# Kernel tuning notes

Hardware: AMD Instinct MI355X
Metric: run time of the kernel (lower is better)

Reference implementation:

```python
import jax, jax.numpy as jnp
import numpy as np
from jax import lax

B, N, D = 16, 4096, 64
NPOINT, RADIUS, NSAMPLE = 1024, 0.2, 32
MLP = [64, 128, 256]
IN_CH = 3 + D
EPS = 1e-5


def farthest_point_sample(xyz, npoint):
    # Deterministic FPS (start at index 0) matching the python fallback loop.
    b, n, _ = xyz.shape

    def step(carry, _):
        dist, farthest = carry
        centroid = jnp.take_along_axis(xyz, farthest[:, None, None], axis=1)  # [B,1,3]
        d = jnp.sum((xyz - centroid) ** 2, axis=-1)  # [B,N]
        dist = jnp.minimum(dist, d)
        nxt = jnp.argmax(dist, axis=-1)
        return (dist, nxt), farthest

    init = (jnp.full((b, n), 1e10, dtype=xyz.dtype), jnp.zeros((b,), jnp.int32))
    _, idx = lax.scan(step, init, None, length=npoint)
    return idx.T  # [B, npoint]


def index_points(points, idx):
    # points: [B,N,C], idx: [B,S] or [B,S,K]
    return jax.vmap(lambda p, i: p[i])(points, idx)


def square_distance(src, dst):
    # src:[B,S,C], dst:[B,N,C] -> [B,S,N]
    d = -2.0 * jnp.einsum('bsc,bnc->bsn', src, dst)
    d += jnp.sum(src ** 2, -1)[:, :, None]
    d += jnp.sum(dst ** 2, -1)[:, None, :]
    return d


def query_ball_point(radius, nsample, xyz, new_xyz):
    b, n, _ = xyz.shape
    sqrdists = square_distance(new_xyz, xyz)  # [B,S,N]
    group_idx = jnp.where(sqrdists > radius ** 2, n, jnp.arange(n, dtype=jnp.int32))
    group_idx = jnp.sort(group_idx, axis=-1)[:, :, :nsample]  # [B,S,K]
    first = group_idx[:, :, :1]
    return jnp.where(group_idx == n, first, group_idx)


def sample_and_group(npoint, radius, nsample, xyz, points):
    fps_idx = farthest_point_sample(xyz, npoint)
    new_xyz = index_points(xyz, fps_idx)  # [B,S,3]
    idx = query_ball_point(radius, nsample, xyz, new_xyz)  # [B,S,K]
    grouped_xyz = index_points(xyz, idx)  # [B,S,K,3]
    grouped_xyz_norm = grouped_xyz - new_xyz[:, :, None, :]
    grouped_points = index_points(points, idx)  # [B,S,K,D]
    new_points = jnp.concatenate([grouped_xyz_norm, grouped_points], axis=-1)
    return new_xyz, new_points


def setup_inputs() -> dict:
    key = jax.random.key(0)
    ks = jax.random.split(key, 2 + 4 * len(MLP))
    inp = {
        'xyz': jax.random.uniform(ks[0], (B, N, 3), jnp.float32),
        'points': jax.random.normal(ks[1], (B, N, D), jnp.float32),
    }
    last = IN_CH
    for i, out in enumerate(MLP):
        kw, kb = ks[2 + 4 * i], ks[3 + 4 * i]
        scale = 1.0 / np.sqrt(last)
        inp[f'w{i}'] = jax.random.normal(kw, (last, out), jnp.float32) * scale
        inp[f'b{i}'] = jax.random.normal(kb, (out,), jnp.float32) * 0.01
        inp[f'g{i}'] = jnp.ones((out,), jnp.float32)
        inp[f'bt{i}'] = jnp.zeros((out,), jnp.float32)
        last = out
    return inp


def _forward(xyz, points, params):
    new_xyz, x = sample_and_group(NPOINT, RADIUS, NSAMPLE, xyz, points)  # x:[B,S,K,C]
    for w, b, g, bt in params:
        x = jnp.einsum('bskc,cd->bskd', x, w) + b  # 1x1 Conv2d
        mean = jnp.mean(x, axis=(0, 1, 2))
        var = jnp.var(x, axis=(0, 1, 2))  # biased, as torch BN training forward
        x = jax.nn.relu((x - mean) * lax.rsqrt(var + EPS) * g + bt)
    new_points = jnp.max(x, axis=2)  # max over nsample -> [B,S,Cout]
    return new_xyz, new_points


def reference(xyz, points, w0, b0, g0, bt0, w1, b1, g1, bt1, w2, b2, g2, bt2):
    params = [(w0, b0, g0, bt0), (w1, b1, g1, bt1), (w2, b2, g2, bt2)]
    return _forward(xyz, points, params)
```

## Files before the change

kernel.cpp:

```cpp
#include <hip/hip_runtime.h>

namespace {
constexpr int kNB = 16;
constexpr int kN  = 4096;
constexpr int kD  = 64;
constexpr int kS  = 1024;
constexpr int kK  = 32;
constexpr int kG  = kNB * kS;
constexpr int C0 = 67, C1 = 64, C2 = 128, C3 = 256;
constexpr float kEps = 1e-5f;
constexpr double kR2d = 0.04000000000000001;
constexpr float kRowCount = (float)(kG * kK);
constexpr int kFT = 256;
constexpr int kFW = kFT / 64;
constexpr int kFP = kN / kFT;
constexpr int kLS = 33;
constexpr int kNF = 88;
}

typedef __attribute__((ext_vector_type(8))) short short8;
typedef __attribute__((ext_vector_type(4))) float f32x4;

__device__ __forceinline__ void split_bf16(float x, unsigned& hi, unsigned& lo) {
  const unsigned u = __float_as_uint(x);
  hi = (u + 0x7fffu + ((u >> 16) & 1u)) >> 16;
  const float rem = x - __uint_as_float(hi << 16);
  const unsigned u2 = __float_as_uint(rem);
  lo = ((u2 + 0x7fffu + ((u2 >> 16) & 1u)) >> 16) & 0xffffu;
}
__device__ __forceinline__ unsigned pack_sb(float x) {
  unsigned hi, lo;
  split_bf16(x, hi, lo);
  return (hi << 16) | lo;
}
__device__ __forceinline__ float unpack_sb(unsigned pk) {
  return __uint_as_float(pk & 0xffff0000u) + __uint_as_float(pk << 16);
}

__device__ __forceinline__ f32x4 mfma3(const short8& ah, const short8& al,
                                       const unsigned short* __restrict__ whiF,
                                       const unsigned short* __restrict__ wloF,
                                       size_t fb, f32x4 acc) {
  const short8 bh = *(const short8*)(whiF + fb);
  const short8 bl = *(const short8*)(wloF + fb);
  acc = __builtin_amdgcn_mfma_f32_16x16x32_bf16(ah, bh, acc, 0, 0, 0);
  acc = __builtin_amdgcn_mfma_f32_16x16x32_bf16(ah, bl, acc, 0, 0, 0);
  acc = __builtin_amdgcn_mfma_f32_16x16x32_bf16(al, bh, acc, 0, 0, 0);
  return acc;
}

__device__ __forceinline__ void load_afrag(const unsigned* p, int k0, int mbase,
                                           int quad, int l15, short8& hi, short8& lo) {
#pragma unroll
  for (int j = 0; j < 8; ++j) {
    const unsigned pk = p[(k0 + quad * 8 + j) * kLS + mbase + l15];
    hi[j] = (short)(pk >> 16);
    lo[j] = (short)(pk & 0xffffu);
  }
}

template <int CTRL, int RM>
__device__ __forceinline__ float dpp_max_step(float v) {
  const int vi = __float_as_int(v);
  const int sh = __builtin_amdgcn_update_dpp(vi, vi, CTRL, RM, 0xf, false);
  return fmaxf(v, __int_as_float(sh));
}
__device__ __forceinline__ float wave_max_dpp(float v) {
  v = dpp_max_step<0x111, 0xf>(v);
  v = dpp_max_step<0x112, 0xf>(v);
  v = dpp_max_step<0x114, 0xf>(v);
  v = dpp_max_step<0x118, 0xf>(v);
  v = dpp_max_step<0x142, 0xa>(v);
  v = dpp_max_step<0x143, 0xc>(v);
  return v;
}

__global__ __launch_bounds__(kFT) void fps_kernel(const float* __restrict__ xyz,
                                                  float* __restrict__ new_xyz) {
#pragma clang fp contract(off)
  const int b = blockIdx.x;
  const int tid = threadIdx.x;
  const int w = tid >> 6;
  const int lane = tid & 63;
  const float* xb = xyz + (size_t)b * kN * 3;

  __shared__ float sx[kN], sy[kN], sz[kN];
  __shared__ float sout[kS * 3];
  __shared__ float4 pV[2];
  __shared__ int4   pI[2];

  float px[kFP], py[kFP], pz[kFP], dist[kFP];
#pragma unroll
  for (int j = 0; j < kFP; ++j) {
    const int p = tid * kFP + j;
    const float x = xb[p * 3 + 0];
    const float y = xb[p * 3 + 1];
    const float z = xb[p * 3 + 2];
    px[j] = x; py[j] = y; pz[j] = z;
    sx[p] = x; sy[p] = y; sz[p] = z;
    dist[j] = 1e10f;
  }
  float cx = xb[0], cy = xb[1], cz = xb[2];
  __syncthreads();

  for (int t = 0; t < kS; ++t) {
    if (tid == 0) {
      sout[t * 3 + 0] = cx; sout[t * 3 + 1] = cy; sout[t * 3 + 2] = cz;
    }
    float lv = -1.0f;
    int bi = 0;
#pragma unroll
    for (int j = 0; j < kFP; ++j) {
      const float dx = px[j] - cx, dy = py[j] - cy, dz = pz[j] - cz;
      float d = dx * dx + dy * dy;
      d = d + dz * dz;
      const float dd = fminf(dist[j], d);
      dist[j] = dd;
      if (dd > lv) { lv = dd; bi = tid * kFP + j; }
    }
    const float wm = wave_max_dpp(lv);
    const float sM = __int_as_float(__builtin_amdgcn_readlane(__float_as_int(wm), 63));
    const unsigned long long mk = __ballot(lv == sM);
    const int fl = __builtin_ctzll(mk);
    const int cand = __builtin_amdgcn_readlane(bi, fl);
    const int par = t & 1;
    if (lane == 0) {
      ((float*)&pV[par])[w] = sM;
      ((int*)&pI[par])[w] = cand;
    }
    __syncthreads();
    const float4 vv = pV[par];
    const int4 ii = pI[par];
    float bv = vv.x; int bci = ii.x;
    if (vv.y > bv) { bv = vv.y; bci = ii.y; }
    if (vv.z > bv) { bv = vv.z; bci = ii.z; }
    if (vv.w > bv) { bv = vv.w; bci = ii.w; }
    cx = sx[bci]; cy = sy[bci]; cz = sz[bci];
  }
  __syncthreads();
  float* ob = new_xyz + (size_t)b * kS * 3;
  for (int e = tid; e < kS * 3; e += kFT) ob[e] = sout[e];
}

__global__ __launch_bounds__(256) void ball_kernel(const float* __restrict__ xyz,
                                                   const float* __restrict__ new_xyz,
                                                   int* __restrict__ idx) {
  const int g = blockIdx.x * 4 + (threadIdx.x >> 6);
  const int lane = threadIdx.x & 63;
  const int b = g >> 10;
  const float* xb = xyz + (size_t)b * kN * 3;
  const double sx = (double)new_xyz[(size_t)g * 3 + 0];
  const double sy = (double)new_xyz[(size_t)g * 3 + 1];
  const double sz = (double)new_xyz[(size_t)g * 3 + 2];
  const double s2 = sx * sx + sy * sy + sz * sz;
  int have = 0, first = -1;
  int* out = idx + (size_t)g * kK;
  for (int c = 0; c < kN; c += 64) {
    const int p = c + lane;
    const double px = (double)xb[p * 3 + 0];
    const double py = (double)xb[p * 3 + 1];
    const double pz = (double)xb[p * 3 + 2];
    const double p2 = px * px + py * py + pz * pz;
    const double dot = sx * px + sy * py + sz * pz;
    const double d = -2.0 * dot + s2 + p2;
    const bool elig = !(d > kR2d);
    const unsigned long long mask = __ballot(elig);
    if (first < 0 && mask) first = c + __builtin_ctzll(mask);
    const int pos = have + __popcll(mask & ((1ull << lane) - 1ull));
    if (elig && pos < kK) out[pos] = p;
    have += __popcll(mask);
    if (have >= kK) break;
  }
  if (have < kK) {
    if (lane >= have && lane < kK) out[lane] = first;
  }
}

__global__ __launch_bounds__(256) void wsplit_kernel(const float* __restrict__ w0,
                                                     const float* __restrict__ w1,
                                                     const float* __restrict__ w2,
                                                     unsigned short* __restrict__ whiF,
                                                     unsigned short* __restrict__ wloF) {
  const int gid = blockIdx.x * 256 + threadIdx.x;
  const int lane = gid & 63;
  const int f = gid >> 6;
  const int quad = lane >> 4, l15 = lane & 15;
  const float* src;
  int kt, nt, nstride;
  if (f < 8) { src = w0; kt = f >> 2; nt = f & 3; nstride = C1; }
  else if (f < 24) { const int fl = f - 8; src = w1; kt = fl >> 3; nt = fl & 7; nstride = C2; }
  else { const int fl = f - 24; src = w2; kt = fl >> 4; nt = fl & 15; nstride = C3; }
  const int k0 = kt * 32 + quad * 8;
  const int n = nt * 16 + l15;
#pragma unroll
  for (int j = 0; j < 8; ++j) {
    const float x = src[(size_t)(k0 + j) * nstride + n];
    unsigned hi, lo;
    split_bf16(x, hi, lo);
    whiF[(size_t)gid * 8 + j] = (unsigned short)hi;
    wloF[(size_t)gid * 8 + j] = (unsigned short)lo;
  }
}

__device__ __forceinline__ void gather_packed(int g, const float* __restrict__ xyz,
                                              const float* __restrict__ points,
                                              const float* __restrict__ new_xyz,
                                              const int* __restrict__ idx,
                                              unsigned* fsp) {
  const int b = g >> 10;
  const float* xb = xyz + (size_t)b * kN * 3;
  const float* pb = points + (size_t)b * kN * kD;
  const float nx = new_xyz[(size_t)g * 3 + 0];
  const float ny = new_xyz[(size_t)g * 3 + 1];
  const float nz = new_xyz[(size_t)g * 3 + 2];
  const int* ig = idx + (size_t)g * kK;
  for (int e = threadIdx.x; e < C0 * kK; e += 256) {
    const int c = e >> 5, r = e & 31;
    const int i = ig[r];
    float v;
    if (c == 0) v = xb[i * 3 + 0] - nx;
    else if (c == 1) v = xb[i * 3 + 1] - ny;
    else if (c == 2) v = xb[i * 3 + 2] - nz;
    else v = pb[(size_t)i * kD + (c - 3)];
    fsp[c * kLS + r] = pack_sb(v);
  }
}

__device__ __forceinline__ void l1_mfma(const unsigned* fsp,
                                        const unsigned short* __restrict__ whiF,
                                        const unsigned short* __restrict__ wloF,
                                        const float* __restrict__ w0,
                                        const float* __restrict__ b0,
                                        int mt, int nh, int quad, int l15, int lane,
                                        f32x4 out[2]) {
  short8 ah[2], al[2];
#pragma unroll
  for (int ks = 0; ks < 2; ++ks)
    load_afrag(fsp, ks * 32, mt * 16, quad, l15, ah[ks], al[ks]);
#pragma unroll
  for (int nt2 = 0; nt2 < 2; ++nt2) {
    const int nt = nh * 2 + nt2;
    const int n = nt * 16 + l15;
    f32x4 acc = {0.f, 0.f, 0.f, 0.f};
#pragma unroll
    for (int ks = 0; ks < 2; ++ks)
      acc = mfma3(ah[ks], al[ks], whiF, wloF, ((size_t)(ks * 4 + nt) * 64 + lane) * 8, acc);
#pragma unroll
    for (int c = 64; c < 67; ++c) {
      const float wv0 = w0[(size_t)c * C1 + n];
#pragma unroll
      for (int r = 0; r < 4; ++r) {
        const float x = unpack_sb(fsp[c * kLS + mt * 16 + quad * 4 + r]);
        acc[r] += x * wv0;
      }
    }
    const float bb = b0[n];
#pragma unroll
    for (int r = 0; r < 4; ++r) acc[r] += bb;
    out[nt2] = acc;
  }
}

__global__ __launch_bounds__(256) void stats1_kernel(
    const float* __restrict__ xyz, const float* __restrict__ points,
    const float* __restrict__ new_xyz, const int* __restrict__ idx,
    const float* __restrict__ w0, const float* __restrict__ b0,
    const unsigned short* __restrict__ whiF, const unsigned short* __restrict__ wloF,
    float* __restrict__ P) {
  __shared__ unsigned fsp[C0 * kLS];
  __shared__ float redS[C1 * 2], redQ[C1 * 2];
  const int g = blockIdx.x;
  const int tid = threadIdx.x;
  gather_packed(g, xyz, points, new_xyz, idx, fsp);
  __syncthreads();
  const int wv = tid >> 6, lane = tid & 63;
  const int mt = wv & 1, nh = wv >> 1;
  const int quad = lane >> 4, l15 = lane & 15;
  f32x4 acc1[2];
  l1_mfma(fsp, whiF, wloF, w0, b0, mt, nh, quad, l15, lane, acc1);
#pragma unroll
  for (int nt2 = 0; nt2 < 2; ++nt2) {
    const int n = (nh * 2 + nt2) * 16 + l15;
    const f32x4 a = acc1[nt2];
    float s = a[0] + a[1] + a[2] + a[3];
    float q = a[0] * a[0] + a[1] * a[1] + a[2] * a[2] + a[3] * a[3];
    s += __shfl_xor(s, 16); s += __shfl_xor(s, 32);
    q += __shfl_xor(q, 16); q += __shfl_xor(q, 32);
    if (quad == 0) { redS[n * 2 + mt] = s; redQ[n * 2 + mt] = q; }
  }
  __syncthreads();
  if (tid < C1) {
    P[(size_t)g * 2 * C1 + tid] = redS[tid * 2] + redS[tid * 2 + 1];
    P[(size_t)g * 2 * C1 + C1 + tid] = redQ[tid * 2] + redQ[tid * 2 + 1];
  }
}

__global__ __launch_bounds__(256) void stats2_kernel(
    const float* __restrict__ xyz, const float* __restrict__ points,
    const float* __restrict__ new_xyz, const int* __restrict__ idx,
    const float* __restrict__ w0, const float* __restrict__ b0, const float* __restrict__ ab0,
    const float* __restrict__ b1,
    const unsigned short* __restrict__ whiF, const unsigned short* __restrict__ wloF,
    float* __restrict__ P) {
  __shared__ unsigned fsp[C0 * kLS];
  __shared__ unsigned y1p[C1 * kLS];
  __shared__ float redS[C2 * 2], redQ[C2 * 2];
  const int g = blockIdx.x;
  const int tid = threadIdx.x;
  gather_packed(g, xyz, points, new_xyz, idx, fsp);
  __syncthreads();
  const int wv = tid >> 6, lane = tid & 63;
  const int mt = wv & 1, nh = wv >> 1;
  const int quad = lane >> 4, l15 = lane & 15;
  {
    f32x4 acc1[2];
    l1_mfma(fsp, whiF, wloF, w0, b0, mt, nh, quad, l15, lane, acc1);
#pragma unroll
    for (int nt2 = 0; nt2 < 2; ++nt2) {
      const int n = (nh * 2 + nt2) * 16 + l15;
      const float a = ab0[n * 2 + 0], c = ab0[n * 2 + 1];
#pragma unroll
      for (int r = 0; r < 4; ++r) {
        const float y = fmaxf(acc1[nt2][r] * a + c, 0.f);
        y1p[n * kLS + mt * 16 + quad * 4 + r] = pack_sb(y);
      }
    }
  }
  __syncthreads();
  {
    short8 ah[2], al[2];
#pragma unroll
    for (int ks = 0; ks < 2; ++ks)
      load_afrag(y1p, ks * 32, mt * 16, quad, l15, ah[ks], al[ks]);
#pragma unroll
    for (int nt2 = 0; nt2 < 4; ++nt2) {
      const int nt = nh * 4 + nt2;
      const int n = nt * 16 + l15;
      f32x4 acc = {0.f, 0.f, 0.f, 0.f};
#pragma unroll
      for (int ks = 0; ks < 2; ++ks)
        acc = mfma3(ah[ks], al[ks], whiF, wloF, ((size_t)(8 + ks * 8 + nt) * 64 + lane) * 8, acc);
      const float bb = b1[n];
      const float v0 = acc[0] + bb, v1 = acc[1] + bb, v2 = acc[2] + bb, v3 = acc[3] + bb;
      float s = v0 + v1 + v2 + v3;
      float q = v0 * v0 + v1 * v1 + v2 * v2 + v3 * v3;
      s += __shfl_xor(s, 16); s += __shfl_xor(s, 32);
      q += __shfl_xor(q, 16); q += __shfl_xor(q, 32);
      if (quad == 0) { redS[n * 2 + mt] = s; redQ[n * 2 + mt] = q; }
    }
  }
  __syncthreads();
  if (tid < C2) {
    P[(size_t)g * 2 * C2 + tid] = redS[tid * 2] + redS[tid * 2 + 1];
    P[(size_t)g * 2 * C2 + C2 + tid] = redQ[tid * 2] + redQ[tid * 2 + 1];
  }
}

__global__ __launch_bounds__(256) void stats3_kernel(
    const float* __restrict__ xyz, const float* __restrict__ points,
    const float* __restrict__ new_xyz, const int* __restrict__ idx,
    const float* __restrict__ w0, const float* __restrict__ b0, const float* __restrict__ ab0,
    const float* __restrict__ b1, const float* __restrict__ ab1,
    const float* __restrict__ b2,
    const unsigned short* __restrict__ whiF, const unsigned short* __restrict__ wloF,
    float* __restrict__ P, float* __restrict__ maxv, float* __restrict__ minv) {
  __shared__ unsigned fsp[C0 * kLS];
  __shared__ unsigned y1p[C1 * kLS];
  __shared__ unsigned y2p[C2 * kLS];
  __shared__ float redS[C3 * 2], redQ[C3 * 2], redM[C3 * 2], redN[C3 * 2];
  const int g = blockIdx.x;
  const int tid = threadIdx.x;
  gather_packed(g, xyz, points, new_xyz, idx, fsp);
  __syncthreads();
  const int wv = tid >> 6, lane = tid & 63;
  const int mt = wv & 1, nh = wv >> 1;
  const int quad = lane >> 4, l15 = lane & 15;
  {
    f32x4 acc1[2];
    l1_mfma(fsp, whiF, wloF, w0, b0, mt, nh, quad, l15, lane, acc1);
#pragma unroll
    for (int nt2 = 0; nt2 < 2; ++nt2) {
      const int n = (nh * 2 + nt2) * 16 + l15;
      const float a = ab0[n * 2 + 0], c = ab0[n * 2 + 1];
#pragma unroll
      for (int r = 0; r < 4; ++r) {
        const float y = fmaxf(acc1[nt2][r] * a + c, 0.f);
        y1p[n * kLS + mt * 16 + quad * 4 + r] = pack_sb(y);
      }
    }
  }
  __syncthreads();
  {
    short8 ah[2], al[2];
#pragma unroll
    for (int ks = 0; ks < 2; ++ks)
      load_afrag(y1p, ks * 32, mt * 16, quad, l15, ah[ks], al[ks]);
#pragma unroll
    for (int nt2 = 0; nt2 < 4; ++nt2) {
      const int nt = nh * 4 + nt2;
      const int n = nt * 16 + l15;
      f32x4 acc = {0.f, 0.f, 0.f, 0.f};
#pragma unroll
      for (int ks = 0; ks < 2; ++ks)
        acc = mfma3(ah[ks], al[ks], whiF, wloF, ((size_t)(8 + ks * 8 + nt) * 64 + lane) * 8, acc);
      const float bb = b1[n];
      const float a = ab1[n * 2 + 0], c = ab1[n * 2 + 1];
#pragma unroll
      for (int r = 0; r < 4; ++r) {
        const float y = fmaxf((acc[r] + bb) * a + c, 0.f);
        y2p[n * kLS + mt * 16 + quad * 4 + r] = pack_sb(y);
      }
    }
  }
  __syncthreads();
  {
    short8 ah[4], al[4];
#pragma unroll
    for (int ks = 0; ks < 4; ++ks)
      load_afrag(y2p, ks * 32, mt * 16, quad, l15, ah[ks], al[ks]);
#pragma unroll
    for (int nt2 = 0; nt2 < 8; ++nt2) {
      const int nt = nh * 8 + nt2;
      f32x4 acc = {0.f, 0.f, 0.f, 0.f};
#pragma unroll
      for (int ks = 0; ks < 4; ++ks)
        acc = mfma3(ah[ks], al[ks], whiF, wloF, ((size_t)(24 + ks * 16 + nt) * 64 + lane) * 8, acc);
      const int n = nt * 16 + l15;
      const float bn = b2[n];
      const float v0 = acc[0] + bn, v1 = acc[1] + bn, v2 = acc[2] + bn, v3 = acc[3] + bn;
      float s = v0 + v1 + v2 + v3;
      float q = v0 * v0 + v1 * v1 + v2 * v2 + v3 * v3;
      float mx = fmaxf(fmaxf(v0, v1), fmaxf(v2, v3));
      float mn = fminf(fminf(v0, v1), fminf(v2, v3));
      s += __shfl_xor(s, 16); s += __shfl_xor(s, 32);
      q += __shfl_xor(q, 16); q += __shfl_xor(q, 32);
      mx = fmaxf(mx, __shfl_xor(mx, 16)); mx = fmaxf(mx, __shfl_xor(mx, 32));
      mn = fminf(mn, __shfl_xor(mn, 16)); mn = fminf(mn, __shfl_xor(mn, 32));
      if (quad == 0) {
        redS[n * 2 + mt] = s; redQ[n * 2 + mt] = q;
        redM[n * 2 + mt] = mx; redN[n * 2 + mt] = mn;
      }
    }
  }
  __syncthreads();
  {
    const int ch = tid;
    P[(size_t)g * 2 * C3 + ch] = redS[ch * 2] + redS[ch * 2 + 1];
    P[(size_t)g * 2 * C3 + C3 + ch] = redQ[ch * 2] + redQ[ch * 2 + 1];
    maxv[(size_t)g * C3 + ch] = fmaxf(redM[ch * 2], redM[ch * 2 + 1]);
    minv[(size_t)g * C3 + ch] = fminf(redN[ch * 2], redN[ch * 2 + 1]);
  }
}

__global__ __launch_bounds__(256) void reduce_kernel(const float* __restrict__ P, int CH,
                                                     const float* __restrict__ gamma,
                                                     const float* __restrict__ beta,
                                                     float* __restrict__ ab) {
  const int ch = blockIdx.x;
  float s = 0.f, q = 0.f;
  for (int i = threadIdx.x; i < kG; i += 256) {
    s += P[(size_t)i * 2 * CH + ch];
    q += P[(size_t)i * 2 * CH + CH + ch];
  }
#pragma unroll
  for (int off = 32; off > 0; off >>= 1) {
    s += __shfl_down(s, off);
    q += __shfl_down(q, off);
  }
  __shared__ float ss[4], qs[4];
  if ((threadIdx.x & 63) == 0) { ss[threadIdx.x >> 6] = s; qs[threadIdx.x >> 6] = q; }
  __syncthreads();
  if (threadIdx.x == 0) {
    s = ss[0] + ss[1] + ss[2] + ss[3];
    q = qs[0] + qs[1] + qs[2] + qs[3];
    const float mean = s / kRowCount;
    float var = q / kRowCount - mean * mean;
    var = fmaxf(var, 0.f);
    const float a = gamma[ch] * (1.0f / sqrtf(var + kEps));
    const float c = beta[ch] - mean * a;
    ab[ch * 2 + 0] = a;
    ab[ch * 2 + 1] = c;
  }
}

__global__ __launch_bounds__(256) void final_kernel(const float* __restrict__ ab2,
                                                    const float* __restrict__ maxv,
                                                    const float* __restrict__ minv,
                                                    float* __restrict__ out) {
  const int e = blockIdx.x * 256 + threadIdx.x;
  const int ch = e & (C3 - 1);
  const float a = ab2[ch * 2 + 0];
  const float c = ab2[ch * 2 + 1];
  const float m = (a >= 0.f) ? maxv[e] : minv[e];
  out[e] = fmaxf(a * m + c, 0.f);
}

extern "C" void kernel_launch(void* const* d_in, const int* in_sizes, int n_in,
                              void* d_out, int out_size, void* d_ws, size_t ws_size,
                              hipStream_t stream) {
  const float* xyz = (const float*)d_in[0];
  const float* points = (const float*)d_in[1];
  const float* w0 = (const float*)d_in[2];
  const float* b0 = (const float*)d_in[3];
  const float* g0 = (const float*)d_in[4];
  const float* bt0 = (const float*)d_in[5];
  const float* w1 = (const float*)d_in[6];
  const float* b1 = (const float*)d_in[7];
  const float* g1 = (const float*)d_in[8];
  const float* bt1 = (const float*)d_in[9];
  const float* w2 = (const float*)d_in[10];
  const float* b2 = (const float*)d_in[11];
  const float* g2 = (const float*)d_in[12];
  const float* bt2 = (const float*)d_in[13];

  float* out_xyz = (float*)d_out;
  float* out_pts = out_xyz + (size_t)kG * 3;

  char* ws = (char*)d_ws;
  int* idx = (int*)ws;
  float* P = (float*)(ws + (size_t)kG * kK * sizeof(int));
  float* maxv = P + (size_t)kG * 2 * C3;
  float* minv = maxv + (size_t)kG * C3;
  float* ab0 = minv + (size_t)kG * C3;
  float* ab1 = ab0 + 2 * C1;
  float* ab2 = ab1 + 2 * C2;
  unsigned short* whiF = (unsigned short*)(ab2 + 2 * C3);
  unsigned short* wloF = whiF + (size_t)kNF * 512;

  wsplit_kernel<<<kNF / 4, 256, 0, stream>>>(w0, w1, w2, whiF, wloF);
  fps_kernel<<<kNB, kFT, 0, stream>>>(xyz, out_xyz);
  ball_kernel<<<kG / 4, 256, 0, stream>>>(xyz, out_xyz, idx);
  stats1_kernel<<<kG, 256, 0, stream>>>(xyz, points, out_xyz, idx, w0, b0, whiF, wloF, P);
  reduce_kernel<<<C1, 256, 0, stream>>>(P, C1, g0, bt0, ab0);
  stats2_kernel<<<kG, 256, 0, stream>>>(xyz, points, out_xyz, idx, w0, b0, ab0, b1,
                                        whiF, wloF, P);
  reduce_kernel<<<C2, 256, 0, stream>>>(P, C2, g1, bt1, ab1);
  stats3_kernel<<<kG, 256, 0, stream>>>(xyz, points, out_xyz, idx, w0, b0, ab0,
                                        b1, ab1, b2, whiF, wloF, P, maxv, minv);
  reduce_kernel<<<C3, 256, 0, stream>>>(P, C3, g2, bt2, ab2);
  final_kernel<<<(kG * C3) / 256, 256, 0, stream>>>(ab2, maxv, minv, out_pts);
}
```

Measured before the change: 1.436 ms.

## Persist layer-2 pre-activations to workspace and vectorize gather loads

stats2 now writes the layer-2 pre-BN outputs, packed as split bf16, to a workspace buffer of 16384x4096 words (256 MB). A new stats3p kernel reads that buffer, applies BN1 and ReLU, and runs only the layer-3 MFMA, so it no longer redoes the gather and the layer-1 and layer-2 matmuls. The gather also switches to float4 loads of point features. The cost is a large extra global write and read, and the new path only runs when the workspace is big enough; otherwise it falls back to the old stats3.

Result: faster. 1.296 ms (-9.8%).

```diff
diff --git a/kernel.cpp b/kernel.cpp
--- a/kernel.cpp
+++ b/kernel.cpp
@@ -15,6 +15,7 @@
 constexpr int kFW = kFT / 64;
 constexpr int kFP = kN / kFT;
 constexpr int kLS = 33;
+constexpr int kXS = 132;
 constexpr int kNF = 88;
 }
 
@@ -210,18 +211,24 @@
   const int b = g >> 10;
   const float* xb = xyz + (size_t)b * kN * 3;
   const float* pb = points + (size_t)b * kN * kD;
-  const float nx = new_xyz[(size_t)g * 3 + 0];
-  const float ny = new_xyz[(size_t)g * 3 + 1];
-  const float nz = new_xyz[(size_t)g * 3 + 2];
   const int* ig = idx + (size_t)g * kK;
-  for (int e = threadIdx.x; e < C0 * kK; e += 256) {
-    const int c = e >> 5, r = e & 31;
+  const int tid = threadIdx.x;
+#pragma unroll
+  for (int it = 0; it < 2; ++it) {
+    const int e = tid + it * 256;
+    const int r = e >> 4, c4 = e & 15;
     const int i = ig[r];
-    float v;
-    if (c == 0) v = xb[i * 3 + 0] - nx;
-    else if (c == 1) v = xb[i * 3 + 1] - ny;
-    else if (c == 2) v = xb[i * 3 + 2] - nz;
-    else v = pb[(size_t)i * kD + (c - 3)];
+    const float4 v = *(const float4*)(pb + (size_t)i * kD + c4 * 4);
+    const int cb = 3 + c4 * 4;
+    fsp[(cb + 0) * kLS + r] = pack_sb(v.x);
+    fsp[(cb + 1) * kLS + r] = pack_sb(v.y);
+    fsp[(cb + 2) * kLS + r] = pack_sb(v.z);
+    fsp[(cb + 3) * kLS + r] = pack_sb(v.w);
+  }
+  if (tid < 96) {
+    const int c = tid >> 5, r = tid & 31;
+    const int i = ig[r];
+    const float v = xb[i * 3 + c] - new_xyz[(size_t)g * 3 + c];
     fsp[c * kLS + r] = pack_sb(v);
   }
 }
@@ -301,9 +308,10 @@
     const float* __restrict__ w0, const float* __restrict__ b0, const float* __restrict__ ab0,
     const float* __restrict__ b1,
     const unsigned short* __restrict__ whiF, const unsigned short* __restrict__ wloF,
-    float* __restrict__ P) {
+    float* __restrict__ P, unsigned* __restrict__ x2p) {
   __shared__ unsigned fsp[C0 * kLS];
   __shared__ unsigned y1p[C1 * kLS];
+  __shared__ unsigned x2s[32 * kXS];
   __shared__ float redS[C2 * 2], redQ[C2 * 2];
   const int g = blockIdx.x;
   const int tid = threadIdx.x;
@@ -342,6 +350,13 @@
         acc = mfma3(ah[ks], al[ks], whiF, wloF, ((size_t)(8 + ks * 8 + nt) * 64 + lane) * 8, acc);
       const float bb = b1[n];
       const float v0 = acc[0] + bb, v1 = acc[1] + bb, v2 = acc[2] + bb, v3 = acc[3] + bb;
+      if (x2p) {
+        const int m0 = mt * 16 + quad * 4;
+        x2s[(m0 + 0) * kXS + n] = pack_sb(v0);
+        x2s[(m0 + 1) * kXS + n] = pack_sb(v1);
+        x2s[(m0 + 2) * kXS + n] = pack_sb(v2);
+        x2s[(m0 + 3) * kXS + n] = pack_sb(v3);
+      }
       float s = v0 + v1 + v2 + v3;
       float q = v0 * v0 + v1 * v1 + v2 * v2 + v3 * v3;
       s += __shfl_xor(s, 16); s += __shfl_xor(s, 32);
@@ -350,6 +365,14 @@
     }
   }
   __syncthreads();
+  if (x2p) {
+#pragma unroll
+    for (int i = 0; i < 16; ++i) {
+      const int f = tid + i * 256;
+      const int m = f >> 7, n = f & 127;
+      x2p[(size_t)g * 4096 + f] = x2s[m * kXS + n];
+    }
+  }
   if (tid < C2) {
     P[(size_t)g * 2 * C2 + tid] = redS[tid * 2] + redS[tid * 2 + 1];
     P[(size_t)g * 2 * C2 + C2 + tid] = redQ[tid * 2] + redQ[tid * 2 + 1];
@@ -452,6 +475,70 @@
   }
 }
 
+__global__ __launch_bounds__(256) void stats3p_kernel(
+    const unsigned* __restrict__ x2p, const float* __restrict__ ab1,
+    const float* __restrict__ b2,
+    const unsigned short* __restrict__ whiF, const unsigned short* __restrict__ wloF,
+    float* __restrict__ P, float* __restrict__ maxv, float* __restrict__ minv) {
+  __shared__ unsigned y2p[C2 * kLS];
+  __shared__ float sab[2 * C2];
+  __shared__ float redS[C3 * 2], redQ[C3 * 2], redM[C3 * 2], redN[C3 * 2];
+  const int g = blockIdx.x;
+  const int tid = threadIdx.x;
+  sab[tid] = ab1[tid];
+  __syncthreads();
+#pragma unroll
+  for (int i = 0; i < 16; ++i) {
+    const int f = tid + i * 256;
+    const int m = f >> 7, n = f & 127;
+    const unsigned pk = x2p[(size_t)g * 4096 + f];
+    const float x = unpack_sb(pk);
+    const float y = fmaxf(x * sab[n * 2 + 0] + sab[n * 2 + 1], 0.f);
+    y2p[n * kLS + m] = pack_sb(y);
+  }
+  __syncthreads();
+  const int wv = tid >> 6, lane = tid & 63;
+  const int mt = wv & 1, nh = wv >> 1;
+  const int quad = lane >> 4, l15 = lane & 15;
+  {
+    short8 ah[4], al[4];
+#pragma unroll
+    for (int ks = 0; ks < 4; ++ks)
+      load_afrag(y2p, ks * 32, mt * 16, quad, l15, ah[ks], al[ks]);
+#pragma unroll
+    for (int nt2 = 0; nt2 < 8; ++nt2) {
+      const int nt = nh * 8 + nt2;
+      f32x4 acc = {0.f, 0.f, 0.f, 0.f};
+#pragma unroll
+      for (int ks = 0; ks < 4; ++ks)
+        acc = mfma3(ah[ks], al[ks], whiF, wloF, ((size_t)(24 + ks * 16 + nt) * 64 + lane) * 8, acc);
+      const int n = nt * 16 + l15;
+      const float bn = b2[n];
+      const float v0 = acc[0] + bn, v1 = acc[1] + bn, v2 = acc[2] + bn, v3 = acc[3] + bn;
+      float s = v0 + v1 + v2 + v3;
+      float q = v0 * v0 + v1 * v1 + v2 * v2 + v3 * v3;
+      float mx = fmaxf(fmaxf(v0, v1), fmaxf(v2, v3));
+      float mn = fminf(fminf(v0, v1), fminf(v2, v3));
+      s += __shfl_xor(s, 16); s += __shfl_xor(s, 32);
+      q += __shfl_xor(q, 16); q += __shfl_xor(q, 32);
+      mx = fmaxf(mx, __shfl_xor(mx, 16)); mx = fmaxf(mx, __shfl_xor(mx, 32));
+      mn = fminf(mn, __shfl_xor(mn, 16)); mn = fminf(mn, __shfl_xor(mn, 32));
+      if (quad == 0) {
+        redS[n * 2 + mt] = s; redQ[n * 2 + mt] = q;
+        redM[n * 2 + mt] = mx; redN[n * 2 + mt] = mn;
+      }
+    }
+  }
+  __syncthreads();
+  {
+    const int ch = tid;
+    P[(size_t)g * 2 * C3 + ch] = redS[ch * 2] + redS[ch * 2 + 1];
+    P[(size_t)g * 2 * C3 + C3 + ch] = redQ[ch * 2] + redQ[ch * 2 + 1];
+    maxv[(size_t)g * C3 + ch] = fmaxf(redM[ch * 2], redM[ch * 2 + 1]);
+    minv[(size_t)g * C3 + ch] = fminf(redN[ch * 2], redN[ch * 2 + 1]);
+  }
+}
+
 __global__ __launch_bounds__(256) void reduce_kernel(const float* __restrict__ P, int CH,
                                                      const float* __restrict__ gamma,
                                                      const float* __restrict__ beta,
@@ -526,6 +613,10 @@
   float* ab2 = ab1 + 2 * C2;
   unsigned short* whiF = (unsigned short*)(ab2 + 2 * C3);
   unsigned short* wloF = whiF + (size_t)kNF * 512;
+  unsigned* x2p = (unsigned*)(wloF + (size_t)kNF * 512);
+  const size_t needed = (size_t)((char*)(x2p + (size_t)kG * 4096) - ws);
+  const bool persist = ws_size >= needed;
+  unsigned* x2arg = persist ? x2p : nullptr;
 
   wsplit_kernel<<<kNF / 4, 256, 0, stream>>>(w0, w1, w2, whiF, wloF);
   fps_kernel<<<kNB, kFT, 0, stream>>>(xyz, out_xyz);
@@ -533,10 +624,14 @@
   stats1_kernel<<<kG, 256, 0, stream>>>(xyz, points, out_xyz, idx, w0, b0, whiF, wloF, P);
   reduce_kernel<<<C1, 256, 0, stream>>>(P, C1, g0, bt0, ab0);
   stats2_kernel<<<kG, 256, 0, stream>>>(xyz, points, out_xyz, idx, w0, b0, ab0, b1,
-                                        whiF, wloF, P);
+                                        whiF, wloF, P, x2arg);
   reduce_kernel<<<C2, 256, 0, stream>>>(P, C2, g1, bt1, ab1);
-  stats3_kernel<<<kG, 256, 0, stream>>>(xyz, points, out_xyz, idx, w0, b0, ab0,
-                                        b1, ab1, b2, whiF, wloF, P, maxv, minv);
+  if (persist) {
+    stats3p_kernel<<<kG, 256, 0, stream>>>(x2p, ab1, b2, whiF, wloF, P, maxv, minv);
+  } else {
+    stats3_kernel<<<kG, 256, 0, stream>>>(xyz, points, out_xyz, idx, w0, b0, ab0,
+                                          b1, ab1, b2, whiF, wloF, P, maxv, minv);
+  }
   reduce_kernel<<<C3, 256, 0, stream>>>(P, C3, g2, bt2, ab2);
   final_kernel<<<(kG * C3) / 256, 256, 0, stream>>>(ab2, maxv, minv, out_pts);
 }
```
